# Performance work log

Measured on AMD Instinct MI355X. Metric: run time of the kernel, lower is better.

The kernel has to match this reference:

```python
import jax, jax.numpy as jnp
import numpy as np

B, L, DM, H = 2, 2048, 1024, 16
D = DM // H  # head_dim = key_dim = 64


def setup_inputs() -> dict:
    key = jax.random.key(0)
    ks = jax.random.split(key, 6)
    w = 0.02
    return {
        "x": jax.random.normal(ks[0], (B, L, DM), dtype=jnp.float32),
        "wq_attn": jax.random.normal(ks[1], (DM, H * D), dtype=jnp.float32) * w,
        "wk_attn": jax.random.normal(ks[2], (DM, H * D), dtype=jnp.float32) * w,
        "wq_rel": jax.random.normal(ks[3], (DM, H * D), dtype=jnp.float32) * w,
        "wk_rel": jax.random.normal(ks[4], (DM, H * D), dtype=jnp.float32) * w,
        "wo": jax.random.normal(ks[5], (H * D, H * D), dtype=jnp.float32) * w,
    }


def reference(x, wq_attn, wk_attn, wq_rel, wk_rel, wo):
    b, l, dm = x.shape
    # projections -> (B, L, H, D); MHA so n_kv_heads == n_heads, no repeat_kv
    q = (x @ wq_attn).reshape(b, l, H, D)
    k = (x @ wk_attn).reshape(b, l, H, D)
    qr = (x @ wq_rel).reshape(b, l, H, D)
    kr = (x @ wk_rel).reshape(b, l, H, D)

    scale = D ** -0.5  # SDPA default: 1/sqrt(query key_dim)
    scores = jnp.einsum("blhd,bmhd->bhlm", q, k) * scale  # (B, H, L, L)
    causal = jnp.tril(jnp.ones((l, l), dtype=bool))
    scores = jnp.where(causal, scores, -jnp.inf)
    attn = jax.nn.softmax(scores, axis=-1)

    # attend over relational keys, then Hadamard with relational queries
    attended_kr = jnp.einsum("bhlm,bmhd->blhd", attn, kr)  # (B, L, H, D)
    attended_relations = qr * attended_kr                    # (B, L, H, D)

    out = attended_relations.reshape(b, l, H * D) @ wo       # (B, L, d_model)
    return out
```

## Files before the change

### kernel.cpp

```cpp
#include <hip/hip_runtime.h>
#include <stdint.h>


typedef __attribute__((ext_vector_type(4))) float floatx4;
typedef __attribute__((ext_vector_type(8))) short shortx8;
typedef __attribute__((ext_vector_type(4))) short shortx4;

__device__ __forceinline__ unsigned short f2bf(float f) {
    unsigned u = __float_as_uint(f);
    u += 0x7fffu + ((u >> 16) & 1u);
    return (unsigned short)(u >> 16);
}
__device__ __forceinline__ float bf2f(unsigned short s) {
    return __uint_as_float(((unsigned)s) << 16);
}
__device__ __forceinline__ float exp2fast(float x) {
#if __has_builtin(__builtin_amdgcn_exp2f)
    return __builtin_amdgcn_exp2f(x);
#else
    return __expf(x * 0.69314718056f);
#endif
}
__device__ __forceinline__ unsigned pkbf(float e0, float e1) {
    return __builtin_amdgcn_perm(__float_as_uint(e1), __float_as_uint(e0), 0x07060302u);
}
__device__ __forceinline__ floatx4 mfma16(shortx4 a, shortx4 b, floatx4 c) {
#if __has_builtin(__builtin_amdgcn_mfma_f32_16x16x16bf16_1k)
    return __builtin_amdgcn_mfma_f32_16x16x16bf16_1k(a, b, c, 0, 0, 0);
#else
    shortx8 a8 = {a[0], a[1], a[2], a[3], 0, 0, 0, 0};
    shortx8 b8 = {b[0], b[1], b[2], b[3], 0, 0, 0, 0};
    return __builtin_amdgcn_mfma_f32_16x16x32_bf16(a8, b8, c, 0, 0, 0);
#endif
}
__device__ __forceinline__ void gll16(const void* g, void* l) {
    __builtin_amdgcn_global_load_lds(
        (const __attribute__((address_space(1))) unsigned int*)g,
        (__attribute__((address_space(3))) unsigned int*)l, 16, 0, 0);
}

__global__ void k_cvt_x(const float* __restrict__ x, unsigned short* __restrict__ xb) {
    int i = (blockIdx.x * 256 + threadIdx.x) * 4;
    float4 v = *(const float4*)(x + i);
    ushort4 o;
    o.x = f2bf(v.x); o.y = f2bf(v.y); o.z = f2bf(v.z); o.w = f2bf(v.w);
    *(ushort4*)(xb + i) = o;
}

__global__ __launch_bounds__(256) void k_cvt_w5(const float* __restrict__ wq,
                                                const float* __restrict__ wk,
                                                const float* __restrict__ wqr,
                                                const float* __restrict__ wkr,
                                                const float* __restrict__ wo,
                                                unsigned short* __restrict__ wcatT,
                                                unsigned short* __restrict__ wotT) {
    __shared__ unsigned short Tl[64 * 65];
    const int t = threadIdx.x;
    const int kt = blockIdx.x * 64, nt = blockIdx.y * 64;
    const int z = blockIdx.z;
    const float* W = (z == 0) ? wq : (z == 1) ? wk : (z == 2) ? wqr : (z == 3) ? wkr : wo;
    unsigned short* outT = (z < 4) ? (wcatT + (size_t)z * 1024 * 1024) : wotT;
    const float scale = (z == 0) ? 0.18033688f : 1.0f;
    {
        const int kl = t >> 3, nc = (t & 7) * 8;
        const float* src = W + (size_t)(kt + kl) * 1024 + nt + nc;
        float a[8], b[8];
        *(float4*)(a)     = *(const float4*)(src);
        *(float4*)(a + 4) = *(const float4*)(src + 4);
        *(float4*)(b)     = *(const float4*)(src + 32 * 1024);
        *(float4*)(b + 4) = *(const float4*)(src + 32 * 1024 + 4);
#pragma unroll
        for (int i = 0; i < 8; ++i) {
            Tl[kl * 65 + nc + i]        = f2bf(a[i] * scale);
            Tl[(kl + 32) * 65 + nc + i] = f2bf(b[i] * scale);
        }
    }
    __syncthreads();
    {
        const int n = t >> 2, kc = (t & 3) * 16;
        shortx8 o0, o1;
#pragma unroll
        for (int i = 0; i < 8; ++i) {
            o0[i] = (short)Tl[(kc + i) * 65 + n];
            o1[i] = (short)Tl[(kc + 8 + i) * 65 + n];
        }
        unsigned short* dst = outT + (size_t)(nt + n) * 1024 + kt + kc;
        *(shortx8*)(dst)     = o0;
        *(shortx8*)(dst + 8) = o1;
    }
}

__global__ __launch_bounds__(512, 1) void k_gemm_bt256(const unsigned short* __restrict__ A,
                                                       const unsigned short* __restrict__ Bt,
                                                       unsigned short* __restrict__ C,
                                                       unsigned short* __restrict__ krT,
                                                       int K) {
    __shared__ alignas(16) unsigned short As[2][256 * 64];
    __shared__ alignas(16) unsigned short Bs[2][256 * 64];
    const int t = threadIdx.x;
    const int lane = t & 63, w = t >> 6;
    const int ln = lane & 15, quad = lane >> 4;
    const int wm = w >> 2, wn = w & 3;
    const int flat = blockIdx.x;
    const int xcd = flat & 7, idx = flat >> 3;
    const int bm = ((xcd >> 1) * 4 + (idx >> 3)) * 256;
    const int bn = ((xcd & 1) * 8 + (idx & 7)) * 256;

    floatx4 acc[8][4] = {};
    shortx8 bfr[4][2];

    const int srow8 = w * 8 + (lane >> 3);
    const int sc8 = (lane & 7) ^ (lane >> 3);
    const unsigned short* gA2 = A + (size_t)(bm + srow8) * K + sc8 * 8;
    const unsigned short* gB2 = Bt + (size_t)(bn + srow8) * K + sc8 * 8;
    const int wb = w * 512;

    auto stA = [&](int kt, int c, int qr) {
        const unsigned short* s = gA2 + (size_t)(qr * 64) * K + kt * 64;
        gll16(s,                   &As[c][(qr * 64) * 64 + wb]);
        gll16(s + (size_t)128 * K, &As[c][(128 + qr * 64) * 64 + wb]);
    };
    auto stB = [&](int kt, int c, int h) {
        const unsigned short* s = gB2 + (size_t)(h * 128) * K + kt * 64;
        gll16(s,                  &Bs[c][(h * 128) * 64 + wb]);
        gll16(s + (size_t)64 * K, &Bs[c][(h * 128 + 64) * 64 + wb]);
    };

    stB(0, 0, 0); stB(0, 0, 1); stA(0, 0, 0); stA(0, 0, 1);
    stB(1, 1, 0); stB(1, 1, 1); stA(1, 1, 0);
    asm volatile("s_waitcnt vmcnt(8)" ::: "memory");
    __builtin_amdgcn_s_barrier();

    const int sl0 = (quad ^ (ln & 7)) * 8;
    const int sl1 = ((4 + quad) ^ (ln & 7)) * 8;

#define GVM(n_) asm volatile("s_waitcnt vmcnt(" #n_ ")" ::: "memory")
#define GLDB(c_)                                                              \
    {                                                                         \
        _Pragma("unroll")                                                     \
        for (int j = 0; j < 4; ++j) {                                         \
            const int br_ = (wn * 64 + j * 16 + ln) * 64;                     \
            bfr[j][0] = *(const shortx8*)(&Bs[c_][br_ + sl0]);                \
            bfr[j][1] = *(const shortx8*)(&Bs[c_][br_ + sl1]);                \
        }                                                                     \
    }
#define GPH(c_, q_, STAGE_STMT, VM_STMT)                                      \
    {                                                                         \
        const int rb_ = (wm * 128 + (q_) * 32 + ln) * 64;                     \
        shortx8 af00 = *(const shortx8*)(&As[c_][rb_ + sl0]);                 \
        shortx8 af01 = *(const shortx8*)(&As[c_][rb_ + sl1]);                 \
        shortx8 af10 = *(const shortx8*)(&As[c_][rb_ + 1024 + sl0]);          \
        shortx8 af11 = *(const shortx8*)(&As[c_][rb_ + 1024 + sl1]);          \
        STAGE_STMT                                                            \
        asm volatile("" ::: "memory");                                        \
        __builtin_amdgcn_s_barrier();                                         \
        asm volatile("s_waitcnt lgkmcnt(0)" ::: "memory");                    \
        __builtin_amdgcn_s_setprio(1);                                        \
        _Pragma("unroll")                                                     \
        for (int j = 0; j < 4; ++j) {                                         \
            acc[(q_)*2][j]   = __builtin_amdgcn_mfma_f32_16x16x32_bf16(af00, bfr[j][0], acc[(q_)*2][j], 0, 0, 0);   \
            acc[(q_)*2][j]   = __builtin_amdgcn_mfma_f32_16x16x32_bf16(af01, bfr[j][1], acc[(q_)*2][j], 0, 0, 0);   \
            acc[(q_)*2+1][j] = __builtin_amdgcn_mfma_f32_16x16x32_bf16(af10, bfr[j][0], acc[(q_)*2+1][j], 0, 0, 0); \
            acc[(q_)*2+1][j] = __builtin_amdgcn_mfma_f32_16x16x32_bf16(af11, bfr[j][1], acc[(q_)*2+1][j], 0, 0, 0); \
        }                                                                     \
        __builtin_amdgcn_s_setprio(0);                                        \
        VM_STMT                                                               \
        asm volatile("" ::: "memory");                                        \
        __builtin_amdgcn_s_barrier();                                         \
    }

    const int NI = K >> 7;
    for (int I = 0; I < NI; ++I) {
        const int n = 2 * I;
        const bool L = (I == NI - 1);
        GLDB(0)
        GPH(0, 0, { stA(n + 1, 1, 1); }, {})
        GPH(0, 1, { if (!L) stB(n + 2, 0, 0); }, { if (L) { GVM(8); } else { GVM(10); } })
        GPH(0, 2, { if (!L) stB(n + 2, 0, 1); }, {})
        GPH(0, 3, { if (!L) stA(n + 2, 0, 0); }, { if (L) { GVM(2); } else { GVM(8); } })
        GLDB(1)
        GPH(1, 0, { if (!L) stA(n + 2, 0, 1); }, {})
        GPH(1, 1, { if (!L) stB(n + 3, 1, 0); }, { if (L) { GVM(0); } else { GVM(10); } })
        GPH(1, 2, { if (!L) stB(n + 3, 1, 1); }, {})
        GPH(1, 3, { if (!L) stA(n + 3, 1, 0); }, { if (!L) { GVM(8); } })
    }
#undef GPH
#undef GLDB
#undef GVM

    if (bn < 3072) {
#pragma unroll
        for (int i = 0; i < 8; ++i)
#pragma unroll
            for (int j = 0; j < 4; ++j)
#pragma unroll
                for (int r = 0; r < 4; ++r) {
                    int row = bm + wm * 128 + i * 16 + quad * 4 + r;
                    int col = bn + wn * 64 + j * 16 + ln;
                    C[(size_t)row * 3072 + col] = f2bf(acc[i][j][r]);
                }
    } else {
        const int b = bm >> 11;
        const int l0b = (bm & 2047) + wm * 128 + quad * 4;
#pragma unroll
        for (int i = 0; i < 8; ++i)
#pragma unroll
            for (int j = 0; j < 4; ++j) {
                const int hd = (bn - 3072) + wn * 64 + j * 16 + ln;
                const int l0 = l0b + i * 16;
                shortx4 o;
#pragma unroll
                for (int r = 0; r < 4; ++r) o[r] = (short)f2bf(acc[i][j][r]);
                *(shortx4*)(krT + ((size_t)(b * 1024 + hd)) * 2048 + l0) = o;
            }
    }
}

__global__ __launch_bounds__(256) void k_gemm_n64(const unsigned short* __restrict__ A,
                                                  const unsigned short* __restrict__ Bt,
                                                  float* __restrict__ C,
                                                  int N, int K) {
    __shared__ alignas(16) unsigned short As[2][128 * 32];
    __shared__ alignas(16) unsigned short Bs[2][64 * 32];
    const int t = threadIdx.x;
    const int lane = t & 63, wv = t >> 6;
    const int ln = lane & 15, quad = lane >> 4;
    const int bm = blockIdx.y * 128, bn = blockIdx.x * 64;

    floatx4 acc[2][4] = {};

    const int srow = t >> 2;
    const int sc = (t & 3) ^ ((srow >> 1) & 3);
    const unsigned short* ga0 = A + (size_t)(bm + srow) * K + sc * 8;
    const unsigned short* ga1 = ga0 + (size_t)64 * K;
    const unsigned short* gb0 = Bt + (size_t)(bn + srow) * K + sc * 8;

    gll16(ga0, &As[0][wv * 512]);
    gll16(ga1, &As[0][2048 + wv * 512]);
    gll16(gb0, &Bs[0][wv * 512]);

    const int sw = (ln >> 1) & 3;
    int cur = 0;
    for (int k0 = 0; k0 < K; k0 += 32, cur ^= 1) {
        __syncthreads();
        const int nk = k0 + 32;
        if (nk < K) {
            gll16(ga0 + nk, &As[cur ^ 1][wv * 512]);
            gll16(ga1 + nk, &As[cur ^ 1][2048 + wv * 512]);
            gll16(gb0 + nk, &Bs[cur ^ 1][wv * 512]);
        }
        shortx8 af[2], bfr[4];
#pragma unroll
        for (int i = 0; i < 2; ++i)
            af[i] = *(const shortx8*)(&As[cur][(wv * 32 + i * 16 + ln) * 32 + ((quad ^ sw) * 8)]);
#pragma unroll
        for (int j = 0; j < 4; ++j)
            bfr[j] = *(const shortx8*)(&Bs[cur][(j * 16 + ln) * 32 + ((quad ^ sw) * 8)]);
#pragma unroll
        for (int i = 0; i < 2; ++i)
#pragma unroll
            for (int j = 0; j < 4; ++j)
                acc[i][j] = __builtin_amdgcn_mfma_f32_16x16x32_bf16(af[i], bfr[j], acc[i][j], 0, 0, 0);
    }

#pragma unroll
    for (int i = 0; i < 2; ++i)
#pragma unroll
        for (int j = 0; j < 4; ++j)
#pragma unroll
            for (int r = 0; r < 4; ++r) {
                int row = bm + wv * 32 + i * 16 + quad * 4 + r;
                int col = bn + j * 16 + ln;
                C[(size_t)row * N + col] = acc[i][j][r];
            }
}

__global__ __launch_bounds__(256, 2) void k_attn(const unsigned short* __restrict__ qcat,
                                                 const unsigned short* __restrict__ krT,
                                                 unsigned short* __restrict__ ar) {
    __shared__ alignas(16) unsigned short Kl[2][64 * 64];
    __shared__ alignas(16) unsigned short Rl[2][64 * 64];
    __shared__ float Ls[4][4][16];

    const int t = threadIdx.x;
    const int lane = t & 63, w = t >> 6;
    const int ln = lane & 15, quad = lane >> 4;
    const int flat = blockIdx.x;
    const int bh = (flat & 7) * 4 + ((flat >> 3) & 3);
    const int qts = flat >> 5;
    const int qt = (qts & 1) ? 31 - (qts >> 1) : (qts >> 1);
    const int b = bh >> 4, h = bh & 15;
    const int l0 = qt * 64;
    const size_t baserow = (size_t)b * 2048;

    shortx8 aq[4][2];
#pragma unroll
    for (int qc = 0; qc < 4; ++qc) {
        const unsigned short* qp =
            qcat + (baserow + l0 + qc * 16 + ln) * 3072 + h * 64 + quad * 8;
        aq[qc][0] = *(const shortx8*)(qp);
        aq[qc][1] = *(const shortx8*)(qp + 32);
    }

    floatx4 acc_o[4][4] = {};
    float lsum[4] = {0.f, 0.f, 0.f, 0.f};

    const int srow = t >> 3;
    const int sc = (t & 7) ^ (srow & 7);
    const unsigned short* gK = qcat + (baserow + srow) * 3072 + 1024 + h * 64 + sc * 8;
    const unsigned short* gR = krT + ((size_t)bh * 64 + srow) * 2048 + sc * 8;

    auto stage = [&](int kt, int buf) {
        gll16(gK + (size_t)(kt * 64) * 3072,      &Kl[buf][w * 512]);
        gll16(gK + (size_t)(kt * 64 + 32) * 3072, &Kl[buf][2048 + w * 512]);
        gll16(gR + kt * 64,                       &Rl[buf][w * 512]);
        gll16(gR + (size_t)32 * 2048 + kt * 64,   &Rl[buf][2048 + w * 512]);
    };

    stage(0, 0);
    const int swz = ln & 7;
    const int krow = (w * 16 + ln) * 64;
    const int cmw = w * 2 + (quad >> 1);
    int cur = 0;
    for (int kt = 0; kt <= qt; ++kt, cur ^= 1) {
        __syncthreads();
        if (kt < qt) stage(kt + 1, cur ^ 1);
        const unsigned short* Kc = Kl[cur];
        const unsigned short* Rc = Rl[cur];
        const bool diag = (kt == qt);

        shortx8 kf0 = *(const shortx8*)(Kc + krow + ((quad ^ swz) * 8));
        shortx8 kf1 = *(const shortx8*)(Kc + krow + (((4 + quad) ^ swz) * 8));
        shortx4 krf[4];
#pragma unroll
        for (int jd = 0; jd < 4; ++jd)
            krf[jd] = *(const shortx4*)(Rc + (jd * 16 + ln) * 64 +
                                        ((cmw ^ swz) * 8) + (quad & 1) * 4);

        const int keyb = kt * 64 + w * 16 + quad * 4;
        shortx4 pk[4];
#pragma unroll
        for (int qc = 0; qc < 4; ++qc) {
            floatx4 z = {0.f, 0.f, 0.f, 0.f};
            z = __builtin_amdgcn_mfma_f32_16x16x32_bf16(kf0, aq[qc][0], z, 0, 0, 0);
            z = __builtin_amdgcn_mfma_f32_16x16x32_bf16(kf1, aq[qc][1], z, 0, 0, 0);
            float e0 = exp2fast(z[0]);
            float e1 = exp2fast(z[1]);
            float e2 = exp2fast(z[2]);
            float e3 = exp2fast(z[3]);
            if (diag) {
                const int q = l0 + qc * 16 + ln;
                e0 = (keyb + 0 > q) ? 0.f : e0;
                e1 = (keyb + 1 > q) ? 0.f : e1;
                e2 = (keyb + 2 > q) ? 0.f : e2;
                e3 = (keyb + 3 > q) ? 0.f : e3;
            }
            lsum[qc] += (e0 + e1) + (e2 + e3);
            struct U2 { unsigned a, b; } u{pkbf(e0, e1), pkbf(e2, e3)};
            pk[qc] = __builtin_bit_cast(shortx4, u);
        }

        __builtin_amdgcn_s_setprio(1);
#pragma unroll
        for (int qc = 0; qc < 4; ++qc)
#pragma unroll
            for (int jd = 0; jd < 4; ++jd)
                acc_o[qc][jd] = mfma16(krf[jd], pk[qc], acc_o[qc][jd]);
        __builtin_amdgcn_s_setprio(0);
    }

#pragma unroll
    for (int qc = 0; qc < 4; ++qc) {
        float s = lsum[qc];
        s += __shfl_xor(s, 16);
        s += __shfl_xor(s, 32);
        lsum[qc] = s;
    }
    if (lane < 16) {
#pragma unroll
        for (int qc = 0; qc < 4; ++qc) Ls[w][qc][lane] = lsum[qc];
    }

    __syncthreads();
    float* redA = (float*)&Kl[0][0];
    float* redB = (float*)&Rl[0][0];
    if (w >= 2) {
        float* dst = (w == 2) ? redA : redB;
#pragma unroll
        for (int qc = 0; qc < 4; ++qc)
#pragma unroll
            for (int jd = 0; jd < 4; ++jd)
                *(floatx4*)(dst + ((qc * 4 + jd) * 64 + lane) * 4) = acc_o[qc][jd];
    }
    __syncthreads();
    if (w < 2) {
        const float* src = (w == 0) ? redA : redB;
#pragma unroll
        for (int qc = 0; qc < 4; ++qc)
#pragma unroll
            for (int jd = 0; jd < 4; ++jd)
                acc_o[qc][jd] += *(const floatx4*)(src + ((qc * 4 + jd) * 64 + lane) * 4);
    }
    __syncthreads();
    if (w == 1) {
#pragma unroll
        for (int qc = 0; qc < 4; ++qc)
#pragma unroll
            for (int jd = 0; jd < 4; ++jd)
                *(floatx4*)(redA + ((qc * 4 + jd) * 64 + lane) * 4) = acc_o[qc][jd];
    }
    __syncthreads();
    if (w == 0) {
        float inv[4];
#pragma unroll
        for (int qc = 0; qc < 4; ++qc)
            inv[qc] = 1.0f / (Ls[0][qc][ln] + Ls[1][qc][ln] + Ls[2][qc][ln] + Ls[3][qc][ln]);
#pragma unroll
        for (int qc = 0; qc < 4; ++qc) {
            const int q = l0 + qc * 16 + ln;
            const unsigned short* qr = qcat + (baserow + q) * 3072 + 2048 + h * 64;
            unsigned short* arow = ar + (baserow + q) * 1024 + h * 64;
#pragma unroll
            for (int jd = 0; jd < 4; ++jd) {
                floatx4 a = acc_o[qc][jd];
                a += *(const floatx4*)(redA + ((qc * 4 + jd) * 64 + lane) * 4);
                const int d0 = jd * 16 + quad * 4;
                shortx4 qv = *(const shortx4*)(qr + d0);
                shortx4 o;
#pragma unroll
                for (int r = 0; r < 4; ++r)
                    o[r] = (short)f2bf(a[r] * inv[qc] * bf2f((unsigned short)qv[r]));
                *(shortx4*)(arow + d0) = o;
            }
        }
    }
}

extern "C" void kernel_launch(void* const* d_in, const int* in_sizes, int n_in,
                              void* d_out, int out_size, void* d_ws, size_t ws_size,
                              hipStream_t stream) {
    const float* x   = (const float*)d_in[0];
    const float* wq  = (const float*)d_in[1];
    const float* wk  = (const float*)d_in[2];
    const float* wqr = (const float*)d_in[3];
    const float* wkr = (const float*)d_in[4];
    const float* wo  = (const float*)d_in[5];
    float* out = (float*)d_out;

    unsigned short* xb    = (unsigned short*)d_ws;
    unsigned short* wcatT = xb + (size_t)4096 * 1024;
    unsigned short* qcat  = wcatT + (size_t)4096 * 1024;
    unsigned short* krT   = qcat + (size_t)4096 * 3072;
    unsigned short* wotT  = krT + (size_t)32 * 64 * 2048;
    unsigned short* arb   = xb;

    k_cvt_x<<<4096, 256, 0, stream>>>(x, xb);
    k_cvt_w5<<<dim3(16, 16, 5), 256, 0, stream>>>(wq, wk, wqr, wkr, wo, wcatT, wotT);
    k_gemm_bt256<<<256, 512, 0, stream>>>(xb, wcatT, qcat, krT, 1024);
    k_attn<<<1024, 256, 0, stream>>>(qcat, krT, arb);
    k_gemm_n64<<<dim3(16, 32), 256, 0, stream>>>(arb, wotT, out, 1024, 1024);
}
```

Measured before the change: 181.7 us.

## Merge conversion kernels and deepen attention K/R prefetch to two tiles ahead

```diff
diff --git a/kernel.cpp b/kernel.cpp
--- a/kernel.cpp
+++ b/kernel.cpp
@@ -39,25 +39,29 @@
         (__attribute__((address_space(3))) unsigned int*)l, 16, 0, 0);
 }
 
-__global__ void k_cvt_x(const float* __restrict__ x, unsigned short* __restrict__ xb) {
-    int i = (blockIdx.x * 256 + threadIdx.x) * 4;
-    float4 v = *(const float4*)(x + i);
-    ushort4 o;
-    o.x = f2bf(v.x); o.y = f2bf(v.y); o.z = f2bf(v.z); o.w = f2bf(v.w);
-    *(ushort4*)(xb + i) = o;
-}
-
-__global__ __launch_bounds__(256) void k_cvt_w5(const float* __restrict__ wq,
-                                                const float* __restrict__ wk,
-                                                const float* __restrict__ wqr,
-                                                const float* __restrict__ wkr,
-                                                const float* __restrict__ wo,
-                                                unsigned short* __restrict__ wcatT,
-                                                unsigned short* __restrict__ wotT) {
+__global__ __launch_bounds__(256) void k_cvt_all(const float* __restrict__ x,
+                                                 const float* __restrict__ wq,
+                                                 const float* __restrict__ wk,
+                                                 const float* __restrict__ wqr,
+                                                 const float* __restrict__ wkr,
+                                                 const float* __restrict__ wo,
+                                                 unsigned short* __restrict__ xb,
+                                                 unsigned short* __restrict__ wcatT,
+                                                 unsigned short* __restrict__ wotT) {
     __shared__ unsigned short Tl[64 * 65];
     const int t = threadIdx.x;
-    const int kt = blockIdx.x * 64, nt = blockIdx.y * 64;
-    const int z = blockIdx.z;
+    if (blockIdx.x < 4096) {
+        int i = (blockIdx.x * 256 + t) * 4;
+        float4 v = *(const float4*)(x + i);
+        ushort4 o;
+        o.x = f2bf(v.x); o.y = f2bf(v.y); o.z = f2bf(v.z); o.w = f2bf(v.w);
+        *(ushort4*)(xb + i) = o;
+        return;
+    }
+    const int zz = blockIdx.x - 4096;
+    const int z = zz >> 8;
+    const int rem = zz & 255;
+    const int kt = (rem & 15) * 64, nt = (rem >> 4) * 64;
     const float* W = (z == 0) ? wq : (z == 1) ? wk : (z == 2) ? wqr : (z == 3) ? wkr : wo;
     unsigned short* outT = (z < 4) ? (wcatT + (size_t)z * 1024 * 1024) : wotT;
     const float scale = (z == 0) ? 0.18033688f : 1.0f;
@@ -318,15 +322,21 @@
     };
 
     stage(0, 0);
+    if (qt >= 1) {
+        stage(1, 1);
+        asm volatile("s_waitcnt vmcnt(4)" ::: "memory");
+    } else {
+        asm volatile("s_waitcnt vmcnt(0)" ::: "memory");
+    }
+    __builtin_amdgcn_s_barrier();
+
     const int swz = ln & 7;
     const int krow = (w * 16 + ln) * 64;
     const int cmw = w * 2 + (quad >> 1);
-    int cur = 0;
-    for (int kt = 0; kt <= qt; ++kt, cur ^= 1) {
-        __syncthreads();
-        if (kt < qt) stage(kt + 1, cur ^ 1);
-        const unsigned short* Kc = Kl[cur];
-        const unsigned short* Rc = Rl[cur];
+    for (int kt = 0; kt <= qt; ++kt) {
+        const int c = kt & 1;
+        const unsigned short* Kc = Kl[c];
+        const unsigned short* Rc = Rl[c];
         const bool diag = (kt == qt);
 
         shortx8 kf0 = *(const shortx8*)(Kc + krow + ((quad ^ swz) * 8));
@@ -336,6 +346,10 @@
         for (int jd = 0; jd < 4; ++jd)
             krf[jd] = *(const shortx4*)(Rc + (jd * 16 + ln) * 64 +
                                         ((cmw ^ swz) * 8) + (quad & 1) * 4);
+        asm volatile("s_waitcnt lgkmcnt(0)" ::: "memory");
+        __builtin_amdgcn_sched_barrier(0);
+        __builtin_amdgcn_s_barrier();
+        if (kt + 2 <= qt) stage(kt + 2, c);
 
         const int keyb = kt * 64 + w * 16 + quad * 4;
         shortx4 pk[4];
@@ -367,6 +381,16 @@
             for (int jd = 0; jd < 4; ++jd)
                 acc_o[qc][jd] = mfma16(krf[jd], pk[qc], acc_o[qc][jd]);
         __builtin_amdgcn_s_setprio(0);
+
+        if (kt + 2 <= qt) {
+            asm volatile("s_waitcnt vmcnt(4)" ::: "memory");
+        } else if (kt + 1 <= qt) {
+            asm volatile("s_waitcnt vmcnt(0)" ::: "memory");
+        }
+        if (kt < qt) {
+            asm volatile("" ::: "memory");
+            __builtin_amdgcn_s_barrier();
+        }
     }
 
 #pragma unroll
@@ -454,8 +478,7 @@
     unsigned short* wotT  = krT + (size_t)32 * 64 * 2048;
     unsigned short* arb   = xb;
 
-    k_cvt_x<<<4096, 256, 0, stream>>>(x, xb);
-    k_cvt_w5<<<dim3(16, 16, 5), 256, 0, stream>>>(wq, wk, wqr, wkr, wo, wcatT, wotT);
+    k_cvt_all<<<5376, 256, 0, stream>>>(x, wq, wk, wqr, wkr, wo, xb, wcatT, wotT);
     k_gemm_bt256<<<256, 512, 0, stream>>>(xb, wcatT, qcat, krT, 1024);
     k_attn<<<1024, 256, 0, stream>>>(qcat, krT, arb);
     k_gemm_n64<<<dim3(16, 32), 256, 0, stream>>>(arb, wotT, out, 1024, 1024);
```

Measured after the change: 189.9 us. +4.5%, slower.
